# Optimization experiments

Measured on AMD Instinct MI355X. Metric: run time of the kernel, lower is better.

## Reference

```python
import jax, jax.numpy as jnp
import numpy as np

N, E, F, DH, R = 50000, 800000, 128, 128, 6  # nodes, edges, in-feat, hidden, relations (heads=1)
EPS = 1e-5
NEG_SLOPE = 0.01


def setup_inputs() -> dict:
    key = jax.random.key(0)
    ks = jax.random.split(key, 20)
    sF = 1.0 / np.sqrt(F)
    sD = 1.0 / np.sqrt(DH)
    return {
        "x": jax.random.normal(ks[0], (N, F), dtype=jnp.float32),
        "edge_index": jax.random.randint(ks[1], (2, E), 0, N, dtype=jnp.int64),
        "edge_type": jax.random.randint(ks[2], (E,), 0, R, dtype=jnp.int64),
        # RGCNConv params
        "rgcn_w": jax.random.normal(ks[3], (R, F, DH), dtype=jnp.float32) * sF,
        "rgcn_root": jax.random.normal(ks[4], (F, DH), dtype=jnp.float32) * sF,
        "rgcn_bias": jnp.zeros((DH,), dtype=jnp.float32),
        # TransformerConv params (heads=1, concat=True)
        "wq": jax.random.normal(ks[5], (DH, DH), dtype=jnp.float32) * sD,
        "bq": jnp.zeros((DH,), dtype=jnp.float32),
        "wk": jax.random.normal(ks[6], (DH, DH), dtype=jnp.float32) * sD,
        "bk": jnp.zeros((DH,), dtype=jnp.float32),
        "wv": jax.random.normal(ks[7], (DH, DH), dtype=jnp.float32) * sD,
        "bv": jnp.zeros((DH,), dtype=jnp.float32),
        "wskip": jax.random.normal(ks[8], (DH, DH), dtype=jnp.float32) * sD,
        "bskip": jnp.zeros((DH,), dtype=jnp.float32),
        # BatchNorm1d params (training-mode batch stats)
        "bn_gamma": jnp.ones((DH,), dtype=jnp.float32),
        "bn_beta": jnp.zeros((DH,), dtype=jnp.float32),
    }


def _rgcn(x, src, dst, edge_type, w, root, bias):
    # PyG RGCNConv: per-relation mean aggregation of x_j @ W_r over incoming edges, + root + bias
    out = x @ root + bias  # [N, DH]
    for r in range(R):
        m = (edge_type == r)
        xw = x @ w[r]  # [N, DH]
        msg = jnp.where(m[:, None], xw[src], 0.0)  # [E, DH]
        s = jax.ops.segment_sum(msg, dst, num_segments=N)
        cnt = jax.ops.segment_sum(m.astype(x.dtype), dst, num_segments=N)
        out = out + s / jnp.maximum(cnt, 1.0)[:, None]
    return out


def _transformer_conv(x, src, dst, wq, bq, wk, bk, wv, bv, wskip, bskip):
    # PyG TransformerConv, heads=1: edge-softmax attention over incoming edges + skip projection
    q = x @ wq + bq  # [N, DH]
    k = x @ wk + bk
    v = x @ wv + bv
    score = jnp.sum(q[dst] * k[src], axis=-1) / jnp.sqrt(jnp.asarray(DH, x.dtype))  # [E]
    smax = jax.ops.segment_max(score, dst, num_segments=N)  # -inf for empty segments (unused)
    a = jnp.exp(score - smax[dst])
    denom = jax.ops.segment_sum(a, dst, num_segments=N)
    alpha = a / denom[dst]  # every edge's dst has >=1 edge, denom > 0
    agg = jax.ops.segment_sum(alpha[:, None] * v[src], dst, num_segments=N)  # [N, DH]
    return agg + (x @ wskip + bskip)


def reference(x, edge_index, edge_type, rgcn_w, rgcn_root, rgcn_bias,
              wq, bq, wk, bk, wv, bv, wskip, bskip, bn_gamma, bn_beta):
    src, dst = edge_index[0], edge_index[1]
    h = _rgcn(x, src, dst, edge_type, rgcn_w, rgcn_root, rgcn_bias)
    h = _transformer_conv(h, src, dst, wq, bq, wk, bk, wv, bv, wskip, bskip)
    # BatchNorm1d (training: batch statistics, biased variance)
    mu = jnp.mean(h, axis=0)
    var = jnp.mean(jnp.square(h - mu), axis=0)
    h = bn_gamma * (h - mu) * jax.lax.rsqrt(var + EPS) + bn_beta
    return jnp.where(h > 0, h, NEG_SLOPE * h)
```

## Files before the change

kernel.cpp:

```cpp
#include <hip/hip_runtime.h>
#include <hip/hip_bf16.h>
#include <math.h>

#define FDIM 128
#define NREL 6

typedef _Float16 half8 __attribute__((ext_vector_type(8)));
typedef _Float16 h16x2 __attribute__((ext_vector_type(2)));
typedef float f32x4 __attribute__((ext_vector_type(4)));

#if __has_builtin(__builtin_amdgcn_fdot2)
#define FDOT2(A, B, C) __builtin_amdgcn_fdot2((A), (B), (C), false)
#else
#define FDOT2(A, B, C) ((float)(A)[0] * (float)(B)[0] + ((float)(A)[1] * (float)(B)[1] + (C)))
#endif

static __device__ __forceinline__ unsigned short f2h(float f) {
  union { _Float16 h; unsigned short u; } p; p.h = (_Float16)f; return p.u;
}

__global__ void cvt_x_kernel(const float* __restrict__ x, unsigned short* __restrict__ xh,
                             int n4) {
  int i = blockIdx.x * 256 + threadIdx.x;
  if (i < n4) {
    float4 v = ((const float4*)x)[i];
    union { _Float16 h[4]; uint2 u; } p;
    p.h[0] = (_Float16)v.x; p.h[1] = (_Float16)v.y;
    p.h[2] = (_Float16)v.z; p.h[3] = (_Float16)v.w;
    ((uint2*)xh)[i] = p.u;
  }
}

__global__ void cvt_wr_kernel(const float* __restrict__ root, const float* __restrict__ w,
                              unsigned short* __restrict__ bt) {
  int i = blockIdx.x * 256 + threadIdx.x;
  if (i < 896 * 128) {
    int n = i / 896, kk = i - n * 896;
    float v = (kk < 128) ? root[kk * 128 + n] : w[(long long)(kk - 128) * 128 + n];
    bt[i] = f2h(v);
  }
}

struct WPtrs { const float* W[4]; };
__global__ void cvt_wq_kernel(WPtrs wp, unsigned short* __restrict__ bt) {
  int i = blockIdx.x * 256 + threadIdx.x;
  if (i < 4 * 128 * 128) {
    int z = i >> 14;
    int r = i & 16383;
    int n = r >> 7, kk = r & 127;
    bt[i] = f2h(wp.W[z][kk * 128 + n]);
  }
}

struct GArgs {
  const unsigned short* Ax;
  const unsigned short* Aagg;
  const unsigned short* Bt;
  const float* bias[4];
  unsigned short* qh; unsigned short* kh; unsigned short* vh; float* sk;
  unsigned short* h;
  int M, K;
};

template <int MODE>
__launch_bounds__(256)
__global__ void gemm_mfma(GArgs g) {
  __shared__ unsigned short Ah[64 * 64];
  __shared__ unsigned short Bh[128 * 64];
  const int tid = threadIdx.x;
  const int lane = tid & 63;
  const int wid = tid >> 6;
  const int wm = wid >> 1, wn = wid & 1;
  const int lr = lane & 15, lk = lane >> 4;
  const int m0 = blockIdx.x * 64;
  const int z = (MODE == 1) ? blockIdx.z : 0;
  const unsigned short* Bt = g.Bt + (long long)z * 128 * g.K;
  const int K = g.K;
  const int M = g.M;

  f32x4 acc[2][4];
#pragma unroll
  for (int a = 0; a < 2; ++a)
#pragma unroll
    for (int b = 0; b < 4; ++b) { acc[a][b][0] = 0.f; acc[a][b][1] = 0.f; acc[a][b][2] = 0.f; acc[a][b][3] = 0.f; }

  for (int k0 = 0; k0 < K; k0 += 64) {
    __syncthreads();
#pragma unroll
    for (int p = 0; p < 2; ++p) {
      int idx = tid + 256 * p;
      int r = idx >> 3, c = idx & 7;
      int row = m0 + r; if (row > M - 1) row = M - 1;
      const unsigned short* srcp;
      if (MODE == 0)
        srcp = (k0 < 128) ? (g.Ax + (long long)row * 128 + k0 + c * 8)
                          : (g.Aagg + (long long)row * 768 + (k0 - 128) + c * 8);
      else
        srcp = g.Ax + (long long)row * 128 + k0 + c * 8;
      uint4 u = *(const uint4*)srcp;
      ((uint4*)Ah)[r * 8 + (c ^ (r & 7))] = u;
    }
#pragma unroll
    for (int p = 0; p < 4; ++p) {
      int idx = tid + 256 * p;
      int rn = idx >> 3, c = idx & 7;
      uint4 u = *(const uint4*)(Bt + (long long)rn * K + k0 + c * 8);
      ((uint4*)Bh)[rn * 8 + (c ^ (rn & 7))] = u;
    }
    __syncthreads();
#pragma unroll
    for (int ks = 0; ks < 2; ++ks) {
      half8 a[2], b[4];
#pragma unroll
      for (int fm = 0; fm < 2; ++fm) {
        int row = wm * 32 + fm * 16 + lr;
        a[fm] = *(const half8*)&((uint4*)Ah)[row * 8 + ((ks * 4 + lk) ^ (row & 7))];
      }
#pragma unroll
      for (int fn = 0; fn < 4; ++fn) {
        int col = wn * 64 + fn * 16 + lr;
        b[fn] = *(const half8*)&((uint4*)Bh)[col * 8 + ((ks * 4 + lk) ^ (col & 7))];
      }
#pragma unroll
      for (int fm = 0; fm < 2; ++fm)
#pragma unroll
        for (int fn = 0; fn < 4; ++fn)
          acc[fm][fn] = __builtin_amdgcn_mfma_f32_16x16x32_f16(a[fm], b[fn], acc[fm][fn], 0, 0, 0);
    }
  }

  const float CF = 0.08838834764831845f * 1.4426950408889634f;
  const float* bias = (MODE == 0) ? g.bias[0] : g.bias[z];
#pragma unroll
  for (int fm = 0; fm < 2; ++fm) {
#pragma unroll
    for (int fn = 0; fn < 4; ++fn) {
      int col = wn * 64 + fn * 16 + lr;
      float bv = bias[col];
#pragma unroll
      for (int j = 0; j < 4; ++j) {
        int row = m0 + wm * 32 + fm * 16 + lk * 4 + j;
        if (row < M) {
          float vv = acc[fm][fn][j] + bv;
          long long off = (long long)row * 128 + col;
          if (MODE == 0) {
            g.h[off] = f2h(vv);
          } else {
            if (z == 0) g.qh[off] = f2h(vv * CF);
            else if (z == 1) g.kh[off] = f2h(vv);
            else if (z == 2) g.vh[off] = f2h(vv);
            else g.sk[off] = vv;
          }
        }
      }
    }
  }
}

__global__ void hist_kernel(const int* __restrict__ dst, const int* __restrict__ etype,
                            int* __restrict__ cnt, int E) {
  int e = blockIdx.x * blockDim.x + threadIdx.x;
  if (e < E) atomicAdd(&cnt[dst[e] * NREL + etype[e]], 1);
}

__launch_bounds__(1024)
__global__ void scan1(const int* __restrict__ deg, int* __restrict__ incl,
                      int* __restrict__ part, int n) {
  __shared__ int sh[1024];
  int tid = threadIdx.x;
  int i = blockIdx.x * 1024 + tid;
  sh[tid] = (i < n) ? deg[i] : 0;
  __syncthreads();
  for (int o = 1; o < 1024; o <<= 1) {
    int t = (tid >= o) ? sh[tid - o] : 0;
    __syncthreads();
    sh[tid] += t;
    __syncthreads();
  }
  if (i < n) incl[i] = sh[tid];
  if (tid == 1023) part[blockIdx.x] = sh[1023];
}

__global__ void scan2(int* part, int nb) {
  int lane = threadIdx.x;
  int run = 0;
  for (int b0 = 0; b0 < nb; b0 += 64) {
    int i = b0 + lane;
    int orig = (i < nb) ? part[i] : 0;
    int v = orig;
#pragma unroll
    for (int o = 1; o < 64; o <<= 1) {
      int t = __shfl_up(v, o);
      if (lane >= o) v += t;
    }
    if (i < nb) part[i] = run + v - orig;
    run += __shfl(v, 63);
  }
}

__global__ void scan3(const int* __restrict__ incl, const int* __restrict__ part,
                      int* __restrict__ offs, int n) {
  int i = blockIdx.x * blockDim.x + threadIdx.x;
  if (i < n) {
    offs[i + 1] = incl[i] + part[i >> 10];
    if (i == 0) offs[0] = 0;
  }
}

__global__ void scatter_kernel(const int* __restrict__ src, const int* __restrict__ dst,
                               const int* __restrict__ etype, const int* __restrict__ offs6,
                               int* __restrict__ cur, int* __restrict__ csrc, int E) {
  int e = blockIdx.x * blockDim.x + threadIdx.x;
  if (e < E) {
    int key = dst[e] * NREL + etype[e];
    int p = offs6[key] + atomicAdd(&cur[key], 1);
    csrc[p] = src[e] << 8;
  }
}

__launch_bounds__(256)
__global__ void rgcn_agg(const unsigned short* __restrict__ xh, const int* __restrict__ offs6,
                         const int* __restrict__ csrc,
                         unsigned short* __restrict__ aggh, int N) {
  int node = blockIdx.x * 4 + (threadIdx.x >> 6);
  if (node >= N) return;
  int lane = threadIdx.x & 63;
  const char* xc = (const char*)xh;
  const int* bp = offs6 + node * NREL;
  const int b0 = bp[0];
  int bn0 = bp[1], bn1 = bp[2], bn2 = bp[3], bn3 = bp[4], bn4 = bp[5], bn5 = bp[6];
  const int b6 = bn5;
  unsigned* ap = (unsigned*)(aggh + (long long)node * (NREL * FDIM)) + lane;

  float tx = 0.f, ty = 0.f;
  float px = 0.f, py = 0.f;
  int bprev = b0, snaps = 0;

#define FLUSH(EPOS)                                                          \
  while (snaps < NREL && bn0 == (EPOS)) {                                    \
    int cnt_ = (EPOS) - bprev;                                               \
    float inv_ = cnt_ ? 1.f / (float)cnt_ : 0.f;                             \
    union { _Float16 h[2]; unsigned u; } pk_;                                \
    pk_.h[0] = (_Float16)((tx - px) * inv_);                                 \
    pk_.h[1] = (_Float16)((ty - py) * inv_);                                 \
    *ap = pk_.u; ap += 64;                                                   \
    px = tx; py = ty; bprev = (EPOS); ++snaps;                               \
    bn0 = bn1; bn1 = bn2; bn2 = bn3; bn3 = bn4; bn4 = bn5;                   \
  }

#define EAT(XU)                                                              \
  {                                                                          \
    union { unsigned u; _Float16 h[2]; } c_; c_.u = (XU);                    \
    tx += (float)c_.h[0]; ty += (float)c_.h[1];                              \
  }

  FLUSH(b0)
  int e = b0;
  for (; e + 8 <= b6; e += 8) {
    unsigned x0 = ((const unsigned*)(xc + csrc[e + 0]))[lane];
    unsigned x1 = ((const unsigned*)(xc + csrc[e + 1]))[lane];
    unsigned x2 = ((const unsigned*)(xc + csrc[e + 2]))[lane];
    unsigned x3 = ((const unsigned*)(xc + csrc[e + 3]))[lane];
    unsigned x4 = ((const unsigned*)(xc + csrc[e + 4]))[lane];
    unsigned x5 = ((const unsigned*)(xc + csrc[e + 5]))[lane];
    unsigned x6 = ((const unsigned*)(xc + csrc[e + 6]))[lane];
    unsigned x7 = ((const unsigned*)(xc + csrc[e + 7]))[lane];
    EAT(x0) FLUSH(e + 1)
    EAT(x1) FLUSH(e + 2)
    EAT(x2) FLUSH(e + 3)
    EAT(x3) FLUSH(e + 4)
    EAT(x4) FLUSH(e + 5)
    EAT(x5) FLUSH(e + 6)
    EAT(x6) FLUSH(e + 7)
    EAT(x7) FLUSH(e + 8)
  }
  for (; e < b6; ++e) {
    unsigned xv = ((const unsigned*)(xc + csrc[e]))[lane];
    EAT(xv) FLUSH(e + 1)
  }
#undef EAT
#undef FLUSH
}

__launch_bounds__(256)
__global__ void attn_kernel(const unsigned short* __restrict__ qh,
                            const unsigned short* __restrict__ kh,
                            const unsigned short* __restrict__ vh,
                            const int* __restrict__ offs6, const int* __restrict__ csrc,
                            float* __restrict__ out, int N) {
  int node = blockIdx.x * 4 + (threadIdx.x >> 6);
  if (node >= N) return;
  int lane = threadIdx.x & 63;
  int start = offs6[node * NREL], end = offs6[node * NREL + NREL];
  int deg = end - start;
  if (deg <= 0) return;

  const int g16 = lane >> 4;
  const int f = lane & 15;
  const char* kc = (const char*)kh;
  const char* vc = (const char*)vh;

  union U4 { uint4 u; h16x2 h[4]; };
  U4 qf; qf.u = *(const uint4*)(qh + (long long)node * FDIM + f * 8);

  float m = -INFINITY, den = 0.f, acc0 = 0.f, acc1 = 0.f;

#define LOADQ(E0, S0, S1, S2, S3, KU, V0, V1, V2, V3)                        \
  {                                                                          \
    S0 = csrc[(E0) + (g16 ^ 0)];                                             \
    S1 = csrc[(E0) + (g16 ^ 1)];                                             \
    S2 = csrc[(E0) + (g16 ^ 2)];                                             \
    S3 = csrc[(E0) + (g16 ^ 3)];                                             \
    KU = *(const uint4*)(kc + S0 + f * 16);                                  \
    V0 = ((const unsigned*)(vc + S0))[lane];                                 \
    V1 = ((const unsigned*)(vc + S1))[lane];                                 \
    V2 = ((const unsigned*)(vc + S2))[lane];                                 \
    V3 = ((const unsigned*)(vc + S3))[lane];                                 \
  }

#define PROCESS(KU, V0, V1, V2, V3, MASKED, M0, M1, M2, M3)                  \
  {                                                                          \
    U4 kf; kf.u = KU;                                                        \
    float pd = FDOT2(qf.h[0], kf.h[0], 0.f);                                 \
    pd = FDOT2(qf.h[1], kf.h[1], pd);                                        \
    pd = FDOT2(qf.h[2], kf.h[2], pd);                                        \
    pd = FDOT2(qf.h[3], kf.h[3], pd);                                        \
    pd += __shfl_xor(pd, 1);  pd += __shfl_xor(pd, 2);                       \
    pd += __shfl_xor(pd, 4);  pd += __shfl_xor(pd, 8);                       \
    float sc0 = pd;                                        \
    float sc1 = __shfl_xor(pd, 16);                        \
    float sc2 = __shfl_xor(pd, 32);                        \
    float sc3 = __shfl_xor(pd, 48);                        \
    if (MASKED) {                                                            \
      if (!(M0)) sc0 = -INFINITY;                                            \
      if (!(M1)) sc1 = -INFINITY;                                            \
      if (!(M2)) sc2 = -INFINITY;                                            \
      if (!(M3)) sc3 = -INFINITY;                                            \
    }                                                                        \
    float mx = fmaxf(fmaxf(sc0, sc1), fmaxf(sc2, sc3));                      \
    float mn = fmaxf(m, mx);                                                 \
    float scl = exp2f(m - mn);                                               \
    float a0 = exp2f(sc0 - mn), a1 = exp2f(sc1 - mn);                        \
    float a2 = exp2f(sc2 - mn), a3 = exp2f(sc3 - mn);                        \
    den = den * scl + ((a0 + a1) + (a2 + a3));                               \
    union { unsigned u; _Float16 h[2]; } w0, w1, w2, w3;                     \
    w0.u = V0; w1.u = V1; w2.u = V2; w3.u = V3;                              \
    acc0 = acc0 * scl + a0 * (float)w0.h[0] + a1 * (float)w1.h[0]            \
                      + a2 * (float)w2.h[0] + a3 * (float)w3.h[0];           \
    acc1 = acc1 * scl + a0 * (float)w0.h[1] + a1 * (float)w1.h[1]            \
                      + a2 * (float)w2.h[1] + a3 * (float)w3.h[1];           \
    m = mn;                                                                  \
  }

  int nfull4 = deg & ~3;
  int e = start;
  if (nfull4 > 0) {
    int sA0, sA1, sA2, sA3; uint4 kA; unsigned vA0, vA1, vA2, vA3;
    LOADQ(e, sA0, sA1, sA2, sA3, kA, vA0, vA1, vA2, vA3)
    for (; e < start + nfull4; e += 4) {
      int sB0, sB1, sB2, sB3; uint4 kB; unsigned vB0, vB1, vB2, vB3;
      bool more = (e + 4 < start + nfull4);
      if (more) LOADQ(e + 4, sB0, sB1, sB2, sB3, kB, vB0, vB1, vB2, vB3)
      PROCESS(kA, vA0, vA1, vA2, vA3, false, 1, 1, 1, 1)
      if (more) { kA = kB; vA0 = vB0; vA1 = vB1; vA2 = vB2; vA3 = vB3; }
    }
  }
  int rem = deg & 3;
  if (rem) {
    int e0 = start + nfull4;
    int j0 = g16 ^ 0, j1 = g16 ^ 1, j2 = g16 ^ 2, j3 = g16 ^ 3;
    int sT0 = csrc[e0 + (j0 < rem ? j0 : 0)];
    int sT1 = csrc[e0 + (j1 < rem ? j1 : 0)];
    int sT2 = csrc[e0 + (j2 < rem ? j2 : 0)];
    int sT3 = csrc[e0 + (j3 < rem ? j3 : 0)];
    uint4 kT = *(const uint4*)(kc + sT0 + f * 16);
    unsigned vT0 = ((const unsigned*)(vc + sT0))[lane];
    unsigned vT1 = ((const unsigned*)(vc + sT1))[lane];
    unsigned vT2 = ((const unsigned*)(vc + sT2))[lane];
    unsigned vT3 = ((const unsigned*)(vc + sT3))[lane];
    PROCESS(kT, vT0, vT1, vT2, vT3, true, j0 < rem, j1 < rem, j2 < rem, j3 < rem)
  }
#undef LOADQ
#undef PROCESS

  float inv = 1.f / den;
  float2* op = (float2*)(out + (long long)node * FDIM);
  float2 o = op[lane];
  o.x += acc0 * inv;
  o.y += acc1 * inv;
  op[lane] = o;
}

__launch_bounds__(128)
__global__ void bn_stats(const float* __restrict__ x, float* __restrict__ gsum,
                         float* __restrict__ gsq, int N) {
  int d = threadIdx.x;
  float s = 0.f, qq = 0.f;
  for (int r = blockIdx.x; r < N; r += gridDim.x) {
    float vv = x[(long long)r * FDIM + d];
    s += vv;
    qq += vv * vv;
  }
  atomicAdd(&gsum[d], s);
  atomicAdd(&gsq[d], qq);
}

__global__ void bn_final(const float* __restrict__ gsum, const float* __restrict__ gsq,
                         const float* __restrict__ gamma, const float* __restrict__ beta,
                         float* __restrict__ ss, int N) {
  int d = threadIdx.x;
  if (d < FDIM) {
    float mean = gsum[d] / (float)N;
    float var = gsq[d] / (float)N - mean * mean;
    var = fmaxf(var, 0.f);
    float sc = gamma[d] * rsqrtf(var + 1e-5f);
    ss[d] = sc;
    ss[FDIM + d] = beta[d] - mean * sc;
  }
}

__global__ void bn_apply(float* __restrict__ x, const float* __restrict__ ss, long long total4) {
  long long i = (long long)blockIdx.x * blockDim.x + threadIdx.x;
  if (i < total4) {
    int d0 = (int)((i * 4) & (FDIM - 1));
    float4 vv = ((const float4*)x)[i];
    float y0 = ss[d0 + 0] * vv.x + ss[FDIM + d0 + 0];
    float y1 = ss[d0 + 1] * vv.y + ss[FDIM + d0 + 1];
    float y2 = ss[d0 + 2] * vv.z + ss[FDIM + d0 + 2];
    float y3 = ss[d0 + 3] * vv.w + ss[FDIM + d0 + 3];
    vv.x = (y0 > 0.f) ? y0 : 0.01f * y0;
    vv.y = (y1 > 0.f) ? y1 : 0.01f * y1;
    vv.z = (y2 > 0.f) ? y2 : 0.01f * y2;
    vv.w = (y3 > 0.f) ? y3 : 0.01f * y3;
    ((float4*)x)[i] = vv;
  }
}

extern "C" void kernel_launch(void* const* d_in, const int* in_sizes, int n_in,
                              void* d_out, int out_size, void* d_ws, size_t ws_size,
                              hipStream_t stream) {
  const float* x         = (const float*)d_in[0];
  const int*   ei        = (const int*)d_in[1];
  const int*   etype     = (const int*)d_in[2];
  const float* rgcn_w    = (const float*)d_in[3];
  const float* rgcn_root = (const float*)d_in[4];
  const float* rgcn_bias = (const float*)d_in[5];
  const float* wq = (const float*)d_in[6];  const float* bq = (const float*)d_in[7];
  const float* wk = (const float*)d_in[8];  const float* bk = (const float*)d_in[9];
  const float* wv = (const float*)d_in[10]; const float* bv = (const float*)d_in[11];
  const float* wsk = (const float*)d_in[12]; const float* bsk = (const float*)d_in[13];
  const float* gamma = (const float*)d_in[14]; const float* beta = (const float*)d_in[15];

  const int N = in_sizes[0] / FDIM;
  const int E = in_sizes[1] / 2;
  const int* src = ei;
  const int* dst = ei + E;
  const int NK = N * NREL;

  char* base = (char*)d_ws;
  size_t off = 0;
  auto alloc = [&](size_t bytes) -> char* {
    char* p = base + off;
    off += (bytes + 255) & ~(size_t)255;
    return p;
  };
  unsigned short* aggh = (unsigned short*)alloc((size_t)N * (NREL * FDIM) * 2);
  unsigned short* qbuf = aggh;
  unsigned short* kbuf = aggh + (size_t)N * FDIM;
  unsigned short* vbuf = aggh + 2 * (size_t)N * FDIM;
  unsigned short* xh   = (unsigned short*)alloc((size_t)N * FDIM * 2);
  unsigned short* hh   = (unsigned short*)alloc((size_t)N * FDIM * 2);
  unsigned short* btR  = (unsigned short*)alloc((size_t)896 * 128 * 2);
  unsigned short* btQ  = (unsigned short*)alloc((size_t)4 * 128 * 128 * 2);
  int* cnt6 = (int*)alloc((size_t)2 * NK * 4);
  int* cur  = cnt6 + NK;
  int* offs6 = (int*)alloc((size_t)(NK + 1) * 4);
  int* incl = (int*)alloc((size_t)NK * 4);
  int* part = (int*)alloc((size_t)512 * 4);
  int* csrc = (int*)alloc((size_t)E * 4);
  float* gsum = (float*)alloc((size_t)(128 + 128 + 256) * 4);
  float* gsq  = gsum + FDIM;
  float* ss   = gsum + 2 * FDIM;

  float* out = (float*)d_out;

  hipMemsetAsync(cnt6, 0, (size_t)2 * NK * sizeof(int), stream);
  hipMemsetAsync(gsum, 0, (size_t)2 * FDIM * sizeof(float), stream);

  int n4 = N * FDIM / 4;
  cvt_x_kernel<<<(n4 + 255) / 256, 256, 0, stream>>>(x, xh, n4);
  cvt_wr_kernel<<<(896 * 128 + 255) / 256, 256, 0, stream>>>(rgcn_root, rgcn_w, btR);
  WPtrs wp; wp.W[0] = wq; wp.W[1] = wk; wp.W[2] = wv; wp.W[3] = wsk;
  cvt_wq_kernel<<<(4 * 128 * 128 + 255) / 256, 256, 0, stream>>>(wp, btQ);

  hist_kernel<<<(E + 255) / 256, 256, 0, stream>>>(dst, etype, cnt6, E);
  int nb = (NK + 1023) / 1024;
  scan1<<<nb, 1024, 0, stream>>>(cnt6, incl, part, NK);
  scan2<<<1, 64, 0, stream>>>(part, nb);
  scan3<<<(NK + 255) / 256, 256, 0, stream>>>(incl, part, offs6, NK);
  scatter_kernel<<<(E + 255) / 256, 256, 0, stream>>>(src, dst, etype, offs6, cur, csrc, E);

  const int nodeBlocks = (N + 3) / 4;
  const int gemmBlocks = (N + 63) / 64;

  rgcn_agg<<<nodeBlocks, 256, 0, stream>>>(xh, offs6, csrc, aggh, N);

  GArgs g0 = {};
  g0.Ax = xh; g0.Aagg = aggh; g0.Bt = btR;
  g0.bias[0] = rgcn_bias;
  g0.h = hh; g0.M = N; g0.K = 896;
  gemm_mfma<0><<<dim3(gemmBlocks, 1, 1), 256, 0, stream>>>(g0);

  GArgs g1 = {};
  g1.Ax = hh; g1.Bt = btQ;
  g1.bias[0] = bq; g1.bias[1] = bk; g1.bias[2] = bv; g1.bias[3] = bsk;
  g1.qh = qbuf; g1.kh = kbuf; g1.vh = vbuf; g1.sk = out;
  g1.M = N; g1.K = 128;
  gemm_mfma<1><<<dim3(gemmBlocks, 1, 4), 256, 0, stream>>>(g1);

  attn_kernel<<<nodeBlocks, 256, 0, stream>>>(qbuf, kbuf, vbuf, offs6, csrc, out, N);

  bn_stats<<<512, 128, 0, stream>>>(out, gsum, gsq, N);
  bn_final<<<1, 128, 0, stream>>>(gsum, gsq, gamma, beta, ss, N);
  long long total4 = (long long)N * FDIM / 4;
  bn_apply<<<(int)((total4 + 255) / 256), 256, 0, stream>>>(out, ss, total4);
}
```

Baseline: 333.1 us.

## Fuse BatchNorm statistics into attention kernel and deepen RGCN gather unroll

The attention kernel now accumulates per-block column sums and sums of squares in shared memory and atomically adds them into 32 bucketed global accumulators. This removes the separate bn_stats pass, which re-read the whole output. bn_final reduces across the buckets. The RGCN aggregation gather loop is also unrolled from 8 to 16 loads, with a 4-wide tail loop. The cost is more atomics, a block-wide barrier in attention, and higher register pressure in the aggregation kernel.

```diff
diff --git a/kernel.cpp b/kernel.cpp
--- a/kernel.cpp
+++ b/kernel.cpp
@@ -256,23 +256,27 @@
 
   FLUSH(b0)
   int e = b0;
-  for (; e + 8 <= b6; e += 8) {
-    unsigned x0 = ((const unsigned*)(xc + csrc[e + 0]))[lane];
-    unsigned x1 = ((const unsigned*)(xc + csrc[e + 1]))[lane];
-    unsigned x2 = ((const unsigned*)(xc + csrc[e + 2]))[lane];
-    unsigned x3 = ((const unsigned*)(xc + csrc[e + 3]))[lane];
-    unsigned x4 = ((const unsigned*)(xc + csrc[e + 4]))[lane];
-    unsigned x5 = ((const unsigned*)(xc + csrc[e + 5]))[lane];
-    unsigned x6 = ((const unsigned*)(xc + csrc[e + 6]))[lane];
-    unsigned x7 = ((const unsigned*)(xc + csrc[e + 7]))[lane];
-    EAT(x0) FLUSH(e + 1)
-    EAT(x1) FLUSH(e + 2)
-    EAT(x2) FLUSH(e + 3)
-    EAT(x3) FLUSH(e + 4)
-    EAT(x4) FLUSH(e + 5)
-    EAT(x5) FLUSH(e + 6)
-    EAT(x6) FLUSH(e + 7)
-    EAT(x7) FLUSH(e + 8)
+  for (; e + 16 <= b6; e += 16) {
+    unsigned xv[16];
+#pragma unroll
+    for (int t = 0; t < 16; ++t)
+      xv[t] = ((const unsigned*)(xc + csrc[e + t]))[lane];
+    EAT(xv[0])  FLUSH(e + 1)   EAT(xv[1])  FLUSH(e + 2)
+    EAT(xv[2])  FLUSH(e + 3)   EAT(xv[3])  FLUSH(e + 4)
+    EAT(xv[4])  FLUSH(e + 5)   EAT(xv[5])  FLUSH(e + 6)
+    EAT(xv[6])  FLUSH(e + 7)   EAT(xv[7])  FLUSH(e + 8)
+    EAT(xv[8])  FLUSH(e + 9)   EAT(xv[9])  FLUSH(e + 10)
+    EAT(xv[10]) FLUSH(e + 11)  EAT(xv[11]) FLUSH(e + 12)
+    EAT(xv[12]) FLUSH(e + 13)  EAT(xv[13]) FLUSH(e + 14)
+    EAT(xv[14]) FLUSH(e + 15)  EAT(xv[15]) FLUSH(e + 16)
+  }
+  for (; e + 4 <= b6; e += 4) {
+    unsigned y0 = ((const unsigned*)(xc + csrc[e + 0]))[lane];
+    unsigned y1 = ((const unsigned*)(xc + csrc[e + 1]))[lane];
+    unsigned y2 = ((const unsigned*)(xc + csrc[e + 2]))[lane];
+    unsigned y3 = ((const unsigned*)(xc + csrc[e + 3]))[lane];
+    EAT(y0) FLUSH(e + 1) EAT(y1) FLUSH(e + 2)
+    EAT(y2) FLUSH(e + 3) EAT(y3) FLUSH(e + 4)
   }
   for (; e < b6; ++e) {
     unsigned xv = ((const unsigned*)(xc + csrc[e]))[lane];
@@ -287,13 +291,17 @@
                             const unsigned short* __restrict__ kh,
                             const unsigned short* __restrict__ vh,
                             const int* __restrict__ offs6, const int* __restrict__ csrc,
-                            float* __restrict__ out, int N) {
-  int node = blockIdx.x * 4 + (threadIdx.x >> 6);
-  if (node >= N) return;
+                            float* __restrict__ out,
+                            float* __restrict__ gsumB, float* __restrict__ gsqB, int N) {
+  __shared__ float bsum[4][FDIM];
+  __shared__ float bsq[4][FDIM];
+  int wv = threadIdx.x >> 6;
+  int node = blockIdx.x * 4 + wv;
   int lane = threadIdx.x & 63;
-  int start = offs6[node * NREL], end = offs6[node * NREL + NREL];
+  bool active = (node < N);
+  int start = 0, end = 0;
+  if (active) { start = offs6[node * NREL]; end = offs6[node * NREL + NREL]; }
   int deg = end - start;
-  if (deg <= 0) return;
 
   const int g16 = lane >> 4;
   const int f = lane & 15;
@@ -301,7 +309,8 @@
   const char* vc = (const char*)vh;
 
   union U4 { uint4 u; h16x2 h[4]; };
-  U4 qf; qf.u = *(const uint4*)(qh + (long long)node * FDIM + f * 8);
+  U4 qf;
+  if (active) qf.u = *(const uint4*)(qh + (long long)node * FDIM + f * 8);
 
   float m = -INFINITY, den = 0.f, acc0 = 0.f, acc1 = 0.f;
 
@@ -327,10 +336,10 @@
     pd = FDOT2(qf.h[3], kf.h[3], pd);                                        \
     pd += __shfl_xor(pd, 1);  pd += __shfl_xor(pd, 2);                       \
     pd += __shfl_xor(pd, 4);  pd += __shfl_xor(pd, 8);                       \
-    float sc0 = pd;                                        \
-    float sc1 = __shfl_xor(pd, 16);                        \
-    float sc2 = __shfl_xor(pd, 32);                        \
-    float sc3 = __shfl_xor(pd, 48);                        \
+    float sc0 = pd;                                                          \
+    float sc1 = __shfl_xor(pd, 16);                                          \
+    float sc2 = __shfl_xor(pd, 32);                                          \
+    float sc3 = __shfl_xor(pd, 48);                                          \
     if (MASKED) {                                                            \
       if (!(M0)) sc0 = -INFINITY;                                            \
       if (!(M1)) sc1 = -INFINITY;                                            \
@@ -352,66 +361,73 @@
     m = mn;                                                                  \
   }
 
-  int nfull4 = deg & ~3;
-  int e = start;
-  if (nfull4 > 0) {
-    int sA0, sA1, sA2, sA3; uint4 kA; unsigned vA0, vA1, vA2, vA3;
-    LOADQ(e, sA0, sA1, sA2, sA3, kA, vA0, vA1, vA2, vA3)
-    for (; e < start + nfull4; e += 4) {
-      int sB0, sB1, sB2, sB3; uint4 kB; unsigned vB0, vB1, vB2, vB3;
-      bool more = (e + 4 < start + nfull4);
-      if (more) LOADQ(e + 4, sB0, sB1, sB2, sB3, kB, vB0, vB1, vB2, vB3)
-      PROCESS(kA, vA0, vA1, vA2, vA3, false, 1, 1, 1, 1)
-      if (more) { kA = kB; vA0 = vB0; vA1 = vB1; vA2 = vB2; vA3 = vB3; }
-    }
-  }
-  int rem = deg & 3;
-  if (rem) {
-    int e0 = start + nfull4;
-    int j0 = g16 ^ 0, j1 = g16 ^ 1, j2 = g16 ^ 2, j3 = g16 ^ 3;
-    int sT0 = csrc[e0 + (j0 < rem ? j0 : 0)];
-    int sT1 = csrc[e0 + (j1 < rem ? j1 : 0)];
-    int sT2 = csrc[e0 + (j2 < rem ? j2 : 0)];
-    int sT3 = csrc[e0 + (j3 < rem ? j3 : 0)];
-    uint4 kT = *(const uint4*)(kc + sT0 + f * 16);
-    unsigned vT0 = ((const unsigned*)(vc + sT0))[lane];
-    unsigned vT1 = ((const unsigned*)(vc + sT1))[lane];
-    unsigned vT2 = ((const unsigned*)(vc + sT2))[lane];
-    unsigned vT3 = ((const unsigned*)(vc + sT3))[lane];
-    PROCESS(kT, vT0, vT1, vT2, vT3, true, j0 < rem, j1 < rem, j2 < rem, j3 < rem)
+  if (deg > 0) {
+    int nfull4 = deg & ~3;
+    int e = start;
+    if (nfull4 > 0) {
+      int sA0, sA1, sA2, sA3; uint4 kA; unsigned vA0, vA1, vA2, vA3;
+      LOADQ(e, sA0, sA1, sA2, sA3, kA, vA0, vA1, vA2, vA3)
+      for (; e < start + nfull4; e += 4) {
+        int sB0, sB1, sB2, sB3; uint4 kB; unsigned vB0, vB1, vB2, vB3;
+        bool more = (e + 4 < start + nfull4);
+        if (more) LOADQ(e + 4, sB0, sB1, sB2, sB3, kB, vB0, vB1, vB2, vB3)
+        PROCESS(kA, vA0, vA1, vA2, vA3, false, 1, 1, 1, 1)
+        if (more) { kA = kB; vA0 = vB0; vA1 = vB1; vA2 = vB2; vA3 = vB3; }
+      }
+    }
+    int rem = deg & 3;
+    if (rem) {
+      int e0 = start + nfull4;
+      int j0 = g16 ^ 0, j1 = g16 ^ 1, j2 = g16 ^ 2, j3 = g16 ^ 3;
+      int sT0 = csrc[e0 + (j0 < rem ? j0 : 0)];
+      int sT1 = csrc[e0 + (j1 < rem ? j1 : 0)];
+      int sT2 = csrc[e0 + (j2 < rem ? j2 : 0)];
+      int sT3 = csrc[e0 + (j3 < rem ? j3 : 0)];
+      uint4 kT = *(const uint4*)(kc + sT0 + f * 16);
+      unsigned vT0 = ((const unsigned*)(vc + sT0))[lane];
+      unsigned vT1 = ((const unsigned*)(vc + sT1))[lane];
+      unsigned vT2 = ((const unsigned*)(vc + sT2))[lane];
+      unsigned vT3 = ((const unsigned*)(vc + sT3))[lane];
+      PROCESS(kT, vT0, vT1, vT2, vT3, true, j0 < rem, j1 < rem, j2 < rem, j3 < rem)
+    }
   }
 #undef LOADQ
 #undef PROCESS
 
-  float inv = 1.f / den;
-  float2* op = (float2*)(out + (long long)node * FDIM);
-  float2 o = op[lane];
-  o.x += acc0 * inv;
-  o.y += acc1 * inv;
-  op[lane] = o;
-}
-
-__launch_bounds__(128)
-__global__ void bn_stats(const float* __restrict__ x, float* __restrict__ gsum,
-                         float* __restrict__ gsq, int N) {
-  int d = threadIdx.x;
-  float s = 0.f, qq = 0.f;
-  for (int r = blockIdx.x; r < N; r += gridDim.x) {
-    float vv = x[(long long)r * FDIM + d];
-    s += vv;
-    qq += vv * vv;
-  }
-  atomicAdd(&gsum[d], s);
-  atomicAdd(&gsq[d], qq);
-}
-
-__global__ void bn_final(const float* __restrict__ gsum, const float* __restrict__ gsq,
+  float2 o = make_float2(0.f, 0.f);
+  if (active) {
+    float2* op = (float2*)(out + (long long)node * FDIM);
+    o = op[lane];
+    if (deg > 0) {
+      float inv = 1.f / den;
+      o.x += acc0 * inv;
+      o.y += acc1 * inv;
+      op[lane] = o;
+    }
+  }
+
+  ((float2*)bsum[wv])[lane] = make_float2(o.x, o.y);
+  ((float2*)bsq[wv])[lane]  = make_float2(o.x * o.x, o.y * o.y);
+  __syncthreads();
+  if (threadIdx.x < FDIM) {
+    int d = threadIdx.x;
+    float s  = bsum[0][d] + bsum[1][d] + bsum[2][d] + bsum[3][d];
+    float q2 = bsq[0][d]  + bsq[1][d]  + bsq[2][d]  + bsq[3][d];
+    int bucket = blockIdx.x & 31;
+    atomicAdd(&gsumB[bucket * FDIM + d], s);
+    atomicAdd(&gsqB[bucket * FDIM + d], q2);
+  }
+}
+
+__global__ void bn_final(const float* __restrict__ gsumB, const float* __restrict__ gsqB,
                          const float* __restrict__ gamma, const float* __restrict__ beta,
                          float* __restrict__ ss, int N) {
   int d = threadIdx.x;
   if (d < FDIM) {
-    float mean = gsum[d] / (float)N;
-    float var = gsq[d] / (float)N - mean * mean;
+    float s = 0.f, q = 0.f;
+    for (int b = 0; b < 32; ++b) { s += gsumB[b * FDIM + d]; q += gsqB[b * FDIM + d]; }
+    float mean = s / (float)N;
+    float var = q / (float)N - mean * mean;
     var = fmaxf(var, 0.f);
     float sc = gamma[d] * rsqrtf(var + 1e-5f);
     ss[d] = sc;
@@ -478,14 +494,14 @@
   int* incl = (int*)alloc((size_t)NK * 4);
   int* part = (int*)alloc((size_t)512 * 4);
   int* csrc = (int*)alloc((size_t)E * 4);
-  float* gsum = (float*)alloc((size_t)(128 + 128 + 256) * 4);
-  float* gsq  = gsum + FDIM;
-  float* ss   = gsum + 2 * FDIM;
+  float* gsumB = (float*)alloc((size_t)32 * FDIM * 4);
+  float* gsqB  = (float*)alloc((size_t)32 * FDIM * 4);
+  float* ss    = (float*)alloc((size_t)2 * FDIM * 4);
 
   float* out = (float*)d_out;
 
   hipMemsetAsync(cnt6, 0, (size_t)2 * NK * sizeof(int), stream);
-  hipMemsetAsync(gsum, 0, (size_t)2 * FDIM * sizeof(float), stream);
+  hipMemsetAsync(gsumB, 0, (size_t)64 * FDIM * sizeof(float), stream);
 
   int n4 = N * FDIM / 4;
   cvt_x_kernel<<<(n4 + 255) / 256, 256, 0, stream>>>(x, xh, n4);
@@ -518,10 +534,10 @@
   g1.M = N; g1.K = 128;
   gemm_mfma<1><<<dim3(gemmBlocks, 1, 4), 256, 0, stream>>>(g1);
 
-  attn_kernel<<<nodeBlocks, 256, 0, stream>>>(qbuf, kbuf, vbuf, offs6, csrc, out, N);
-
-  bn_stats<<<512, 128, 0, stream>>>(out, gsum, gsq, N);
-  bn_final<<<1, 128, 0, stream>>>(gsum, gsq, gamma, beta, ss, N);
+  attn_kernel<<<nodeBlocks, 256, 0, stream>>>(qbuf, kbuf, vbuf, offs6, csrc, out,
+                                              gsumB, gsqB, N);
+
+  bn_final<<<1, 128, 0, stream>>>(gsumB, gsqB, gamma, beta, ss, N);
   long long total4 = (long long)N * FDIM / 4;
   bn_apply<<<(int)((total4 + 255) / 256), 256, 0, stream>>>(out, ss, total4);
 }
```

After: 305.2 us. 1.09x faster.
